# Optimization experiments

Measured on AMD Instinct MI355X. Metric: run time of the kernel, lower is better.

Reference implementation:

```python
import jax, jax.numpy as jnp
import numpy as np

# Graph/batch constants (compressed-edge representation of graph.adjmat)
B, N, E, D = 64, 1024, 1_048_576, 128        # graphs, nodes/graph, edges, new_edge_dim
EDGE_DIM, MSSG_DIM, GLOB_DIM, CNDT_DIM = 64, 32, 8, 8
HIDDEN, N_HEADS = 256, 4
HEAD_DIM = D // N_HEADS                        # 32
ATTN_IN = MSSG_DIM + EDGE_DIM + GLOB_DIM + CNDT_DIM  # 112
NUM_SEG = B * N


def setup_inputs() -> dict:
    key = jax.random.key(0)
    ks = jax.random.split(key, 11)
    new_edges = jax.random.normal(ks[0], (E, D), dtype=jnp.float32)
    edges = jax.random.normal(ks[1], (E, EDGE_DIM), dtype=jnp.float32)
    pooled_mssgs = jax.random.normal(ks[2], (E, MSSG_DIM), dtype=jnp.float32)
    globs = jax.random.normal(ks[3], (B, GLOB_DIM), dtype=jnp.float32)
    cndts = jax.random.normal(ks[4], (B, CNDT_DIM), dtype=jnp.float32)
    W1 = jax.random.normal(ks[5], (ATTN_IN, HIDDEN), dtype=jnp.float32) * (1.0 / np.sqrt(ATTN_IN))
    b1 = jnp.zeros((HIDDEN,), dtype=jnp.float32)
    W2 = jax.random.normal(ks[6], (HIDDEN, N_HEADS), dtype=jnp.float32) * (1.0 / np.sqrt(HIDDEN))
    b2 = jnp.zeros((N_HEADS,), dtype=jnp.float32)
    batch_idx = jnp.sort(jax.random.randint(ks[7], (E,), 0, B, dtype=jnp.int32))
    recv_idx = jax.random.randint(ks[8], (E,), 0, N, dtype=jnp.int32)
    return dict(new_edges=new_edges, edges=edges, pooled_mssgs=pooled_mssgs,
                globs=globs, cndts=cndts, W1=W1, b1=b1, W2=W2, b2=b2,
                batch_idx=batch_idx, recv_idx=recv_idx)


def reference(new_edges, edges, pooled_mssgs, globs, cndts, W1, b1, W2, b2,
              batch_idx, recv_idx):
    # ctxt_from_mask: broadcast per-graph globs/cndts to each compressed edge  [E, g+c]
    ctxt = jnp.concatenate([globs[batch_idx], cndts[batch_idx]], axis=-1)
    # smart_cat([pooled_mssgs, graph.edges]) + ctxt concat inside DenseNetwork
    x = jnp.concatenate([pooled_mssgs, edges, ctxt], axis=-1)      # [E, 112]
    h = jax.nn.leaky_relu(x @ W1 + b1, 0.1)                        # [E, 256]
    logits = h @ W2 + b2                                           # [E, n_heads]

    # segment id = (graph, receiver) slot; adjmat nonzeros -> compressed edges
    seg = batch_idx * N + recv_idx                                 # [E]

    # aggr_via_sparse(..., reduction='softmax', dim=1): masked segment softmax per head
    m = jax.ops.segment_max(logits, seg, num_segments=NUM_SEG)     # [B*N, H]
    ex = jnp.exp(logits - m[seg])
    denom = jax.ops.segment_sum(ex, seg, num_segments=NUM_SEG)
    attn = ex / denom[seg]                                         # [E, H]

    # unsqueeze(-1).expand(-1,-1,head_dim).flatten(1) == repeat each head head_dim times
    w = jnp.repeat(attn, HEAD_DIM, axis=1)                         # [E, D]

    # aggr_via_sparse(..., 'sum', dim=1) then decompress onto dense [B, N, D]
    pooled = jax.ops.segment_sum(new_edges * w, seg, num_segments=NUM_SEG)
    return pooled.reshape(B, N, D)
```

## Files before the change

kernel.cpp:

```cpp
#include <hip/hip_runtime.h>
#include <hip/hip_bf16.h>
#include <cstdint>
#include <cstddef>

#define E_TOT   1048576
#define BGR     64
#define NN      1024
#define DD      128
#define HID     256
#define NH      4
#define NSEG    65536
#define KDIM    96
#define NKCH    12
#define BM      64
#define NTILES  (E_TOT/BM)
#define GRIDM   512
#define TPB     (NTILES/GRIDM)

typedef __attribute__((ext_vector_type(8))) short s16x8;
typedef __attribute__((ext_vector_type(4))) float f32x4;

static __device__ __forceinline__ unsigned short f2bf_rn(float f) {
    unsigned u = __float_as_uint(f);
    unsigned r = u + 0x7FFF + ((u >> 16) & 1);
    return (unsigned short)(r >> 16);
}

__global__ __launch_bounds__(256)
void k_prep_w(const float* __restrict__ W1, short* __restrict__ Wg) {
    int idx = blockIdx.x * 256 + threadIdx.x;
    int kchunk = idx >> 11;
    int n      = (idx >> 3) & 255;
    int j      = idx & 7;
    int k      = kchunk * 8 + j;
    Wg[idx] = (short)f2bf_rn(W1[k * 256 + n]);
}

__global__ __launch_bounds__(256)
void k_prep_ctx(const float* __restrict__ W1, const float* __restrict__ b1,
                const float* __restrict__ globs, const float* __restrict__ cndts,
                float* __restrict__ ctxtc) {
    int b = blockIdx.x, j = threadIdx.x;
    float s = b1[j];
    #pragma unroll
    for (int g = 0; g < 8; ++g) s = fmaf(globs[b * 8 + g], W1[(96 + g) * 256 + j], s);
    #pragma unroll
    for (int c = 0; c < 8; ++c) s = fmaf(cndts[b * 8 + c], W1[(104 + c) * 256 + j], s);
    ctxtc[b * 256 + j] = s;
}

__global__ __launch_bounds__(256)
void k_count(const int* __restrict__ batch_idx, const int* __restrict__ recv_idx,
             int* __restrict__ counts)
{
    int e = blockIdx.x * 256 + threadIdx.x;
    atomicAdd(&counts[batch_idx[e] * NN + recv_idx[e]], 1);
}

__global__ __launch_bounds__(256)
void k_scan1(const int* __restrict__ counts, int* __restrict__ tmp_excl,
             int* __restrict__ blocksums)
{
    __shared__ int sh[256];
    const int t = threadIdx.x;
    const int gid = blockIdx.x * 256 + t;
    int c = counts[gid];
    sh[t] = c;
    __syncthreads();
    int v = c;
    for (int off = 1; off < 256; off <<= 1) {
        int u = (t >= off) ? sh[t - off] : 0;
        __syncthreads();
        v += u; sh[t] = v;
        __syncthreads();
    }
    tmp_excl[gid] = v - c;
    if (t == 255) blocksums[blockIdx.x] = v;
}

__global__ __launch_bounds__(256)
void k_scan2(int* __restrict__ blocksums)
{
    __shared__ int sh[256];
    const int t = threadIdx.x;
    int c = blocksums[t];
    sh[t] = c;
    __syncthreads();
    int v = c;
    for (int off = 1; off < 256; off <<= 1) {
        int u = (t >= off) ? sh[t - off] : 0;
        __syncthreads();
        v += u; sh[t] = v;
        __syncthreads();
    }
    blocksums[t] = v - c;
}

__global__ __launch_bounds__(256)
void k_scan3(const int* __restrict__ tmp_excl, const int* __restrict__ blocksums,
             int* __restrict__ offsets, int* __restrict__ cursor)
{
    const int gid = blockIdx.x * 256 + threadIdx.x;
    int v = tmp_excl[gid] + blocksums[blockIdx.x];
    offsets[gid] = v;
    cursor[gid]  = v;
}

__global__ __launch_bounds__(256)
void k_scatter(const int* __restrict__ batch_idx, const int* __restrict__ recv_idx,
               int* __restrict__ cursor, int* __restrict__ elist)
{
    int e   = blockIdx.x * 256 + threadIdx.x;
    int seg = batch_idx[e] * NN + recv_idx[e];
    int pos = atomicAdd(&cursor[seg], 1);
    elist[pos] = e;
}

__global__ __launch_bounds__(512, 4)
void k_mlp_mfma(const float* __restrict__ pooled, const float* __restrict__ edges,
                const short* __restrict__ Wg,     const float* __restrict__ ctxtc,
                const float* __restrict__ W2,
                const int* __restrict__ batch_idx, const int* __restrict__ recv_idx,
                float* __restrict__ ex_out, float* __restrict__ denom)
{
    __shared__ short Wl[NKCH * 256 * 8];
    __shared__ short Xl[NKCH * BM * 8];
    __shared__ float sW2[256 * 4];
    __shared__ float plog[4][BM][4];

    const int tid  = threadIdx.x;
    const int lane = tid & 63;
    const int wid  = tid >> 6;
    const int la   = lane & 15;
    const int g    = lane >> 4;
    const int es   = wid & 1;
    const int hq   = wid >> 1;

    {
        const float4* src = reinterpret_cast<const float4*>(Wg);
        float4* dst = reinterpret_cast<float4*>(Wl);
        #pragma unroll
        for (int i = 0; i < 6; ++i) dst[i * 512 + tid] = src[i * 512 + tid];
        if (tid < 256)
            *reinterpret_cast<float4*>(&sW2[tid * 4]) =
                reinterpret_cast<const float4*>(W2)[tid];
    }

    const int u0 = tid;
    const int u1 = tid + 512;
    const int e_u0 = u0 / 12, k_u0 = u0 - e_u0 * 12;
    const int e_u1 = u1 / 12, k_u1 = u1 - e_u1 * 12;

    {
        const int e0 = blockIdx.x * TPB * BM;
        {
            const int eg = e0 + e_u0;
            const float* p = (k_u0 < 4) ? (pooled + (size_t)eg * 32 + k_u0 * 8)
                                        : (edges + (size_t)eg * 64 + (k_u0 - 4) * 8);
            float4 v0 = reinterpret_cast<const float4*>(p)[0];
            float4 v1 = reinterpret_cast<const float4*>(p)[1];
            float vals[8] = {v0.x,v0.y,v0.z,v0.w,v1.x,v1.y,v1.z,v1.w};
            s16x8 hv;
            #pragma unroll
            for (int i = 0; i < 8; ++i) hv[i] = (short)f2bf_rn(vals[i]);
            *reinterpret_cast<s16x8*>(&Xl[(k_u0 * BM + e_u0) * 8]) = hv;
        }
        if (tid < 256) {
            const int eg = e0 + e_u1;
            const float* p = (k_u1 < 4) ? (pooled + (size_t)eg * 32 + k_u1 * 8)
                                        : (edges + (size_t)eg * 64 + (k_u1 - 4) * 8);
            float4 v0 = reinterpret_cast<const float4*>(p)[0];
            float4 v1 = reinterpret_cast<const float4*>(p)[1];
            float vals[8] = {v0.x,v0.y,v0.z,v0.w,v1.x,v1.y,v1.z,v1.w};
            s16x8 hv;
            #pragma unroll
            for (int i = 0; i < 8; ++i) hv[i] = (short)f2bf_rn(vals[i]);
            *reinterpret_cast<s16x8*>(&Xl[(k_u1 * BM + e_u1) * 8]) = hv;
        }
    }
    __syncthreads();

    for (int t = 0; t < TPB; ++t) {
        const int e0 = (blockIdx.x * TPB + t) * BM;
        const bool has_next = (t + 1 < TPB);

        float4 sa0, sa1, sb0, sb1;
        if (has_next) {
            const int en = e0 + BM;
            {
                const int eg = en + e_u0;
                const float* p = (k_u0 < 4) ? (pooled + (size_t)eg * 32 + k_u0 * 8)
                                            : (edges + (size_t)eg * 64 + (k_u0 - 4) * 8);
                sa0 = reinterpret_cast<const float4*>(p)[0];
                sa1 = reinterpret_cast<const float4*>(p)[1];
            }
            if (tid < 256) {
                const int eg = en + e_u1;
                const float* p = (k_u1 < 4) ? (pooled + (size_t)eg * 32 + k_u1 * 8)
                                            : (edges + (size_t)eg * 64 + (k_u1 - 4) * 8);
                sb0 = reinterpret_cast<const float4*>(p)[0];
                sb1 = reinterpret_cast<const float4*>(p)[1];
            }
        }

        f32x4 acc[4][2];
        #pragma unroll
        for (int i = 0; i < 4; ++i) {
            acc[i][0] = (f32x4){0.f, 0.f, 0.f, 0.f};
            acc[i][1] = (f32x4){0.f, 0.f, 0.f, 0.f};
        }
        #pragma unroll
        for (int ks = 0; ks < 3; ++ks) {
            const int kb = ks * 4 + g;
            const s16x8 xf0 = *reinterpret_cast<const s16x8*>(
                &Xl[(kb * BM + es * 32 + la) * 8]);
            const s16x8 xf1 = *reinterpret_cast<const s16x8*>(
                &Xl[(kb * BM + es * 32 + 16 + la) * 8]);
            const short* wrow = &Wl[(kb * 256 + hq * 64 + la) * 8];
            #pragma unroll
            for (int hf = 0; hf < 4; ++hf) {
                s16x8 wf = *reinterpret_cast<const s16x8*>(wrow + hf * 128);
                acc[hf][0] = __builtin_amdgcn_mfma_f32_16x16x32_bf16(wf, xf0, acc[hf][0], 0, 0, 0);
                acc[hf][1] = __builtin_amdgcn_mfma_f32_16x16x32_bf16(wf, xf1, acc[hf][1], 0, 0, 0);
            }
        }

        {
            const int ea = e0 + es * 32 + la;
            const int eb = ea + 16;
            const int ba = batch_idx[ea];
            const int bb = batch_idx[eb];
            const float* cxa_base = &ctxtc[(size_t)ba * 256 + hq * 64 + g * 4];
            const float* cxb_base = &ctxtc[(size_t)bb * 256 + hq * 64 + g * 4];
            float pa0 = 0.f, pa1 = 0.f, pa2 = 0.f, pa3 = 0.f;
            float pb0 = 0.f, pb1 = 0.f, pb2 = 0.f, pb3 = 0.f;
            #pragma unroll
            for (int hf = 0; hf < 4; ++hf) {
                const float4 cxa = *reinterpret_cast<const float4*>(cxa_base + hf * 16);
                const float4 cxb = *reinterpret_cast<const float4*>(cxb_base + hf * 16);
                const float cxaa[4] = {cxa.x, cxa.y, cxa.z, cxa.w};
                const float cxba[4] = {cxb.x, cxb.y, cxb.z, cxb.w};
                #pragma unroll
                for (int r = 0; r < 4; ++r) {
                    const int j = hq * 64 + hf * 16 + g * 4 + r;
                    const float4 w2v = *reinterpret_cast<const float4*>(&sW2[j * 4]);
                    float sa = acc[hf][0][r] + cxaa[r];
                    float ha = fmaxf(sa, 0.1f * sa);
                    float sb = acc[hf][1][r] + cxba[r];
                    float hb = fmaxf(sb, 0.1f * sb);
                    pa0 = fmaf(ha, w2v.x, pa0); pb0 = fmaf(hb, w2v.x, pb0);
                    pa1 = fmaf(ha, w2v.y, pa1); pb1 = fmaf(hb, w2v.y, pb1);
                    pa2 = fmaf(ha, w2v.z, pa2); pb2 = fmaf(hb, w2v.z, pb2);
                    pa3 = fmaf(ha, w2v.w, pa3); pb3 = fmaf(hb, w2v.w, pb3);
                }
            }
            pa0 += __shfl_xor(pa0, 16); pa0 += __shfl_xor(pa0, 32);
            pa1 += __shfl_xor(pa1, 16); pa1 += __shfl_xor(pa1, 32);
            pa2 += __shfl_xor(pa2, 16); pa2 += __shfl_xor(pa2, 32);
            pa3 += __shfl_xor(pa3, 16); pa3 += __shfl_xor(pa3, 32);
            pb0 += __shfl_xor(pb0, 16); pb0 += __shfl_xor(pb0, 32);
            pb1 += __shfl_xor(pb1, 16); pb1 += __shfl_xor(pb1, 32);
            pb2 += __shfl_xor(pb2, 16); pb2 += __shfl_xor(pb2, 32);
            pb3 += __shfl_xor(pb3, 16); pb3 += __shfl_xor(pb3, 32);
            float pla = (g == 0) ? pa0 : (g == 1) ? pa1 : (g == 2) ? pa2 : pa3;
            float plb = (g == 0) ? pb0 : (g == 1) ? pb1 : (g == 2) ? pb2 : pb3;
            plog[hq][es * 32 + la][g]      = pla;
            plog[hq][es * 32 + 16 + la][g] = plb;
        }
        __syncthreads();

        if (has_next) {
            {
                float vals[8] = {sa0.x,sa0.y,sa0.z,sa0.w,sa1.x,sa1.y,sa1.z,sa1.w};
                s16x8 hv;
                #pragma unroll
                for (int i = 0; i < 8; ++i) hv[i] = (short)f2bf_rn(vals[i]);
                *reinterpret_cast<s16x8*>(&Xl[(k_u0 * BM + e_u0) * 8]) = hv;
            }
            if (tid < 256) {
                float vals[8] = {sb0.x,sb0.y,sb0.z,sb0.w,sb1.x,sb1.y,sb1.z,sb1.w};
                s16x8 hv;
                #pragma unroll
                for (int i = 0; i < 8; ++i) hv[i] = (short)f2bf_rn(vals[i]);
                *reinterpret_cast<s16x8*>(&Xl[(k_u1 * BM + e_u1) * 8]) = hv;
            }
        }

        if (tid < 256) {
            const int e = tid >> 2;
            const int h = tid & 3;
            const int eg = e0 + e;
            float lg = plog[0][e][h] + plog[1][e][h] + plog[2][e][h] + plog[3][e][h];
            float exv = __expf(lg);
            ex_out[(size_t)eg * 4 + h] = exv;
            const int seg = batch_idx[eg] * NN + recv_idx[eg];
            atomicAdd(&denom[seg * 4 + h], exv);
        }
        __syncthreads();
    }
}

__global__ __launch_bounds__(256)
void k_gather(const float* __restrict__ new_edges, const float* __restrict__ ex,
              const float* __restrict__ denom, const int* __restrict__ offsets,
              const int* __restrict__ counts, const int* __restrict__ elist,
              float* __restrict__ out)
{
    const int gid  = blockIdx.x * 256 + threadIdx.x;
    const int seg  = gid >> 6;
    const int lane = threadIdx.x & 63;
    if (seg >= NSEG) return;

    const int start = offsets[seg];
    const int cnt   = counts[seg];
    const int h     = lane >> 4;
    const int doff  = lane * 2;

    float a0 = 0.f, a1 = 0.f;
    int i = 0;
    for (; i + 4 <= cnt; i += 4) {
        const int el0 = elist[start + i + 0];
        const int el1 = elist[start + i + 1];
        const int el2 = elist[start + i + 2];
        const int el3 = elist[start + i + 3];
        const float w0 = ex[(size_t)el0 * 4 + h];
        const float w1 = ex[(size_t)el1 * 4 + h];
        const float w2 = ex[(size_t)el2 * 4 + h];
        const float w3 = ex[(size_t)el3 * 4 + h];
        const float2 n0 = *reinterpret_cast<const float2*>(new_edges + (size_t)el0 * DD + doff);
        const float2 n1 = *reinterpret_cast<const float2*>(new_edges + (size_t)el1 * DD + doff);
        const float2 n2 = *reinterpret_cast<const float2*>(new_edges + (size_t)el2 * DD + doff);
        const float2 n3 = *reinterpret_cast<const float2*>(new_edges + (size_t)el3 * DD + doff);
        a0 = fmaf(n0.x, w0, a0); a1 = fmaf(n0.y, w0, a1);
        a0 = fmaf(n1.x, w1, a0); a1 = fmaf(n1.y, w1, a1);
        a0 = fmaf(n2.x, w2, a0); a1 = fmaf(n2.y, w2, a1);
        a0 = fmaf(n3.x, w3, a0); a1 = fmaf(n3.y, w3, a1);
    }
    for (; i < cnt; ++i) {
        const int el = elist[start + i];
        const float w = ex[(size_t)el * 4 + h];
        const float2 n = *reinterpret_cast<const float2*>(new_edges + (size_t)el * DD + doff);
        a0 = fmaf(n.x, w, a0); a1 = fmaf(n.y, w, a1);
    }
    const float scale = (cnt > 0) ? 1.0f / denom[seg * 4 + h] : 0.0f;
    float2 r; r.x = a0 * scale; r.y = a1 * scale;
    *reinterpret_cast<float2*>(out + (size_t)seg * DD + doff) = r;
}

extern "C" void kernel_launch(void* const* d_in, const int* in_sizes, int n_in,
                              void* d_out, int out_size, void* d_ws, size_t ws_size,
                              hipStream_t stream)
{
    const float* new_edges = (const float*)d_in[0];
    const float* edges     = (const float*)d_in[1];
    const float* pooled    = (const float*)d_in[2];
    const float* globs     = (const float*)d_in[3];
    const float* cndts     = (const float*)d_in[4];
    const float* W1        = (const float*)d_in[5];
    const float* b1        = (const float*)d_in[6];
    const float* W2        = (const float*)d_in[7];
    const int*   batch_idx = (const int*)d_in[9];
    const int*   recv_idx  = (const int*)d_in[10];
    float* out = (float*)d_out;

    char* ws = (char*)d_ws;
    float* ex       = (float*)(ws);
    float* denom    = (float*)(ws + (size_t)16 * 1024 * 1024);
    char*  base17   = ws + (size_t)17 * 1024 * 1024;
    int*   counts   = (int*)(base17);
    int*   offs     = (int*)(base17 + 1 * 262144);
    int*   cursor   = (int*)(base17 + 2 * 262144);
    int*   tmp_excl = (int*)(base17 + 3 * 262144);
    int*   bsums    = (int*)(base17 + 4 * 262144);
    int*   elist    = (int*)(ws + (size_t)18 * 1024 * 1024);
    short* Wg       = (short*)(ws + (size_t)22 * 1024 * 1024);
    float* ctxtc    = (float*)(ws + (size_t)22 * 1024 * 1024 + 65536);

    hipMemsetAsync(denom, 0,
                   (size_t)NSEG * NH * sizeof(float) + (size_t)NSEG * sizeof(int),
                   stream);

    k_count<<<E_TOT / 256, 256, 0, stream>>>(batch_idx, recv_idx, counts);
    k_scan1<<<NSEG / 256, 256, 0, stream>>>(counts, tmp_excl, bsums);
    k_scan2<<<1, 256, 0, stream>>>(bsums);
    k_scan3<<<NSEG / 256, 256, 0, stream>>>(tmp_excl, bsums, offs, cursor);
    k_scatter<<<E_TOT / 256, 256, 0, stream>>>(batch_idx, recv_idx, cursor, elist);

    k_prep_w<<<96, 256, 0, stream>>>(W1, Wg);
    k_prep_ctx<<<64, 256, 0, stream>>>(W1, b1, globs, cndts, ctxtc);
    k_mlp_mfma<<<GRIDM, 512, 0, stream>>>(pooled, edges, Wg, ctxtc, W2,
                                          batch_idx, recv_idx, ex, denom);

    k_gather<<<(NSEG * 64) / 256, 256, 0, stream>>>(new_edges, ex, denom,
                                                    offs, counts, elist, out);
}
```

Measured before the change: 347.9 us.

## Fuse prep kernels, fold scan2 into scan3, move scatter into MLP kernel

Merges the count, weight-conversion and context-precompute kernels into one launch split by block index. Replaces the separate block-sum scan kernel with a per-block reduction of preceding block sums inside scan3. Folds the edge-list scatter into the MLP epilogue so the segment id computed there is reused. This cuts four kernel launches and one pass over batch_idx/recv_idx, at the cost of redundant block-sum reductions and extra atomics inside the MLP kernel.

```diff
diff --git a/kernel.cpp b/kernel.cpp
--- a/kernel.cpp
+++ b/kernel.cpp
@@ -27,34 +27,33 @@
 }
 
 __global__ __launch_bounds__(256)
-void k_prep_w(const float* __restrict__ W1, short* __restrict__ Wg) {
-    int idx = blockIdx.x * 256 + threadIdx.x;
-    int kchunk = idx >> 11;
-    int n      = (idx >> 3) & 255;
-    int j      = idx & 7;
-    int k      = kchunk * 8 + j;
-    Wg[idx] = (short)f2bf_rn(W1[k * 256 + n]);
-}
-
-__global__ __launch_bounds__(256)
-void k_prep_ctx(const float* __restrict__ W1, const float* __restrict__ b1,
-                const float* __restrict__ globs, const float* __restrict__ cndts,
-                float* __restrict__ ctxtc) {
-    int b = blockIdx.x, j = threadIdx.x;
-    float s = b1[j];
-    #pragma unroll
-    for (int g = 0; g < 8; ++g) s = fmaf(globs[b * 8 + g], W1[(96 + g) * 256 + j], s);
-    #pragma unroll
-    for (int c = 0; c < 8; ++c) s = fmaf(cndts[b * 8 + c], W1[(104 + c) * 256 + j], s);
-    ctxtc[b * 256 + j] = s;
-}
-
-__global__ __launch_bounds__(256)
-void k_count(const int* __restrict__ batch_idx, const int* __restrict__ recv_idx,
-             int* __restrict__ counts)
-{
-    int e = blockIdx.x * 256 + threadIdx.x;
-    atomicAdd(&counts[batch_idx[e] * NN + recv_idx[e]], 1);
+void k_misc(const float* __restrict__ W1, const float* __restrict__ b1,
+            const float* __restrict__ globs, const float* __restrict__ cndts,
+            const int* __restrict__ batch_idx, const int* __restrict__ recv_idx,
+            short* __restrict__ Wg, float* __restrict__ ctxtc,
+            int* __restrict__ counts)
+{
+    const int bid = blockIdx.x;
+    const int tid = threadIdx.x;
+    if (bid < 4096) {
+        int e = bid * 256 + tid;
+        atomicAdd(&counts[batch_idx[e] * NN + recv_idx[e]], 1);
+    } else if (bid < 4096 + 96) {
+        int idx = (bid - 4096) * 256 + tid;
+        int kchunk = idx >> 11;
+        int n      = (idx >> 3) & 255;
+        int j      = idx & 7;
+        int k      = kchunk * 8 + j;
+        Wg[idx] = (short)f2bf_rn(W1[k * 256 + n]);
+    } else {
+        int b = bid - 4192, j = tid;
+        float s = b1[j];
+        #pragma unroll
+        for (int g = 0; g < 8; ++g) s = fmaf(globs[b * 8 + g], W1[(96 + g) * 256 + j], s);
+        #pragma unroll
+        for (int c = 0; c < 8; ++c) s = fmaf(cndts[b * 8 + c], W1[(104 + c) * 256 + j], s);
+        ctxtc[b * 256 + j] = s;
+    }
 }
 
 __global__ __launch_bounds__(256)
@@ -79,41 +78,22 @@
 }
 
 __global__ __launch_bounds__(256)
-void k_scan2(int* __restrict__ blocksums)
-{
-    __shared__ int sh[256];
-    const int t = threadIdx.x;
-    int c = blocksums[t];
-    sh[t] = c;
-    __syncthreads();
-    int v = c;
-    for (int off = 1; off < 256; off <<= 1) {
-        int u = (t >= off) ? sh[t - off] : 0;
-        __syncthreads();
-        v += u; sh[t] = v;
-        __syncthreads();
-    }
-    blocksums[t] = v - c;
-}
-
-__global__ __launch_bounds__(256)
 void k_scan3(const int* __restrict__ tmp_excl, const int* __restrict__ blocksums,
              int* __restrict__ offsets, int* __restrict__ cursor)
 {
-    const int gid = blockIdx.x * 256 + threadIdx.x;
-    int v = tmp_excl[gid] + blocksums[blockIdx.x];
-    offsets[gid] = v;
-    cursor[gid]  = v;
-}
-
-__global__ __launch_bounds__(256)
-void k_scatter(const int* __restrict__ batch_idx, const int* __restrict__ recv_idx,
-               int* __restrict__ cursor, int* __restrict__ elist)
-{
-    int e   = blockIdx.x * 256 + threadIdx.x;
-    int seg = batch_idx[e] * NN + recv_idx[e];
-    int pos = atomicAdd(&cursor[seg], 1);
-    elist[pos] = e;
+    __shared__ int swv[4];
+    const int t = threadIdx.x;
+    const int bid = blockIdx.x;
+    int v = (t < bid) ? blocksums[t] : 0;
+    #pragma unroll
+    for (int off = 1; off < 64; off <<= 1) v += __shfl_xor(v, off);
+    if ((t & 63) == 0) swv[t >> 6] = v;
+    __syncthreads();
+    const int base = swv[0] + swv[1] + swv[2] + swv[3];
+    const int gid = bid * 256 + t;
+    int o = tmp_excl[gid] + base;
+    offsets[gid] = o;
+    cursor[gid]  = o;
 }
 
 __global__ __launch_bounds__(512, 4)
@@ -121,7 +101,8 @@
                 const short* __restrict__ Wg,     const float* __restrict__ ctxtc,
                 const float* __restrict__ W2,
                 const int* __restrict__ batch_idx, const int* __restrict__ recv_idx,
-                float* __restrict__ ex_out, float* __restrict__ denom)
+                float* __restrict__ ex_out, float* __restrict__ denom,
+                int* __restrict__ cursor, int* __restrict__ elist)
 {
     __shared__ short Wl[NKCH * 256 * 8];
     __shared__ short Xl[NKCH * BM * 8];
@@ -295,6 +276,10 @@
             ex_out[(size_t)eg * 4 + h] = exv;
             const int seg = batch_idx[eg] * NN + recv_idx[eg];
             atomicAdd(&denom[seg * 4 + h], exv);
+            if (h == 0) {
+                int pos = atomicAdd(&cursor[seg], 1);
+                elist[pos] = eg;
+            }
         }
         __syncthreads();
     }
@@ -380,16 +365,15 @@
                    (size_t)NSEG * NH * sizeof(float) + (size_t)NSEG * sizeof(int),
                    stream);
 
-    k_count<<<E_TOT / 256, 256, 0, stream>>>(batch_idx, recv_idx, counts);
+    k_misc<<<4096 + 96 + 64, 256, 0, stream>>>(W1, b1, globs, cndts,
+                                               batch_idx, recv_idx,
+                                               Wg, ctxtc, counts);
     k_scan1<<<NSEG / 256, 256, 0, stream>>>(counts, tmp_excl, bsums);
-    k_scan2<<<1, 256, 0, stream>>>(bsums);
     k_scan3<<<NSEG / 256, 256, 0, stream>>>(tmp_excl, bsums, offs, cursor);
-    k_scatter<<<E_TOT / 256, 256, 0, stream>>>(batch_idx, recv_idx, cursor, elist);
-
-    k_prep_w<<<96, 256, 0, stream>>>(W1, Wg);
-    k_prep_ctx<<<64, 256, 0, stream>>>(W1, b1, globs, cndts, ctxtc);
+
     k_mlp_mfma<<<GRIDM, 512, 0, stream>>>(pooled, edges, Wg, ctxtc, W2,
-                                          batch_idx, recv_idx, ex, denom);
+                                          batch_idx, recv_idx, ex, denom,
+                                          cursor, elist);
 
     k_gather<<<(NSEG * 64) / 256, 256, 0, stream>>>(new_edges, ex, denom,
                                                     offs, counts, elist, out);
```

Result: faster. 325.6 us (-6.4%).
